# Performance work log

Hardware: AMD Instinct MI355X
Metric: run time of the kernel (lower is better)

Reference implementation:

```python
import jax, jax.numpy as jnp
import numpy as np

NQ = 6          # num_qubits
BS = 3          # basis_size (Pauli x,y,z)
HID = 32        # LSTM hidden size
SNAPS = 16      # max_num_snapshots
BATCH = 1024
DIM = 2 ** NQ   # 64


def _pauli():
    sx = np.array([[0., 1.], [1., 0.]], dtype=np.complex64)
    sy = np.array([[0., -1j], [1j, 0.]], dtype=np.complex64)
    sz = np.array([[1., 0.], [0., -1.]], dtype=np.complex64)
    return np.stack([sx, sy, sz], axis=0)


def setup_inputs():
    key = jax.random.key(0)
    ks = jax.random.split(key, 12)
    snapshot = jax.random.uniform(ks[0], (BATCH, NQ), jnp.float32, -1.0, 1.0)
    basis_comp_vector = jax.nn.softmax(
        jax.random.normal(ks[1], (BATCH, NQ, BS), jnp.float32), axis=-1)
    # valid density matrices: rho = A A^dag / tr
    ar = jax.random.normal(ks[2], (BATCH, DIM, DIM), jnp.float32)
    ai = jax.random.normal(ks[3], (BATCH, DIM, DIM), jnp.float32)
    A = ar + 1j * ai
    rho_c = jnp.einsum('bij,bkj->bik', A, jnp.conj(A))
    tr = jnp.trace(rho_c, axis1=1, axis2=2)[:, None, None]
    rho_c = rho_c / tr
    rho = jnp.stack([jnp.real(rho_c), jnp.imag(rho_c)], axis=1).astype(jnp.float32)
    h0 = jax.random.normal(ks[4], (BATCH, HID), jnp.float32)
    c0 = jax.random.normal(ks[5], (BATCH, HID), jnp.float32)
    in_dim = NQ + NQ * BS
    W_ih = jax.random.normal(ks[6], (4 * HID, in_dim), jnp.float32) * 0.1
    W_hh = jax.random.normal(ks[7], (4 * HID, HID), jnp.float32) * 0.1
    b_ih = jax.random.normal(ks[8], (4 * HID,), jnp.float32) * 0.05
    b_hh = jax.random.normal(ks[9], (4 * HID,), jnp.float32) * 0.05
    Wp = jax.random.normal(ks[10], (NQ, HID, BS), jnp.float32) * 0.1
    bp = jax.random.normal(ks[11], (NQ, BS), jnp.float32) * 0.05
    pauli = _pauli()
    basis_r = jnp.asarray(np.real(pauli), jnp.float32)
    basis_i = jnp.asarray(np.imag(pauli), jnp.float32)
    return {"snapshot": snapshot, "basis_comp_vector": basis_comp_vector,
            "rho": rho, "h0": h0, "c0": c0,
            "W_ih": W_ih, "W_hh": W_hh, "b_ih": b_ih, "b_hh": b_hh,
            "Wp": Wp, "bp": bp, "basis_r": basis_r, "basis_i": basis_i}


def _apply(p, M, axis, b):
    # apply 2x2 batched operator M [b,2,2] on tensor axis `axis` of p [b]+(2,)*2NQ
    pm = jnp.moveaxis(p, axis, 1)
    shp = pm.shape
    out = jnp.einsum('bij,bjr->bir', M, pm.reshape(b, 2, -1)).reshape(shp)
    return jnp.moveaxis(out, 1, axis)


def _measure(rho_t, probs, basis, basis_c, b):
    # sequential single-qubit measurement on the collapsing mixed state
    pc = probs.astype(jnp.complex64)
    M = jnp.einsum('bqs,sij->bqij', pc, basis)    # prob-mixed basis ops
    Mc = jnp.einsum('bqs,sij->bqij', pc, basis_c)
    p = rho_t
    outs = []
    for q in range(NQ):
        p = _apply(p, M[:, q], 1 + q, b)          # row index of qubit q
        p = _apply(p, Mc[:, q], 1 + NQ + q, b)    # col index of qubit q
        tr = jnp.trace(p.reshape(b, DIM, DIM), axis1=1, axis2=2)
        outs.append(jnp.real(tr))                 # measurement value s
        p = p / tr.reshape((b,) + (1,) * (2 * NQ))  # renormalized post-state
    return jnp.stack(outs, axis=1)                 # [b, NQ]


def _forward(snapshot, basis_comp_vector, rho, h0, c0,
             W_ih, W_hh, b_ih, b_hh, Wp, bp, basis_r, basis_i):
    b = snapshot.shape[0]
    basis = (basis_r + 1j * basis_i).astype(jnp.complex64)
    basis_c = jnp.conj(basis)
    rho_t = (rho[:, 0] + 1j * rho[:, 1]).astype(jnp.complex64)
    rho_t = rho_t.reshape((b,) + (2,) * (2 * NQ))

    x = jnp.concatenate([snapshot, basis_comp_vector.reshape(b, -1)], axis=-1)
    feats = [x]
    h, c = h0, c0
    for _ in range(SNAPS - 1):
        # torch LSTMCell: gate order i, f, g, o
        g = x @ W_ih.T + b_ih + h @ W_hh.T + b_hh
        gi, gf, gg, go = jnp.split(g, 4, axis=-1)
        c = jax.nn.sigmoid(gf) * c + jax.nn.sigmoid(gi) * jnp.tanh(gg)
        h = jax.nn.sigmoid(go) * jnp.tanh(c)
        probs = jax.nn.softmax(jnp.einsum('bh,qhs->bqs', h, Wp) + bp, axis=-1)
        # torch.Tensor(snapshot_batch) detaches -> stop_gradient
        snaps = jax.lax.stop_gradient(_measure(rho_t, probs, basis, basis_c, b))
        x = jnp.concatenate([snaps, probs.reshape(b, -1)], axis=-1)
        feats.append(x)

    # classical-shadow reconstruction: kron_q (I + 3 s_q B_q)/2, averaged
    eye2 = jnp.eye(2, dtype=jnp.complex64)
    acc = jnp.zeros((b, DIM, DIM), jnp.complex64)
    last_bv = None
    for xw in feats:
        shadow = xw[:, :NQ]
        bv = xw[:, NQ:].reshape(b, NQ, BS)
        last_bv = bv
        Bq = jnp.einsum('bqs,sij->bqij', bv.astype(jnp.complex64), basis)
        rc = (eye2 + 3.0 * shadow[:, :, None, None].astype(jnp.complex64) * Bq) / 2.0
        k = rc[:, 0]
        dd = 2
        for q in range(1, NQ):  # batched kron chain
            k = jnp.einsum('bij,bkl->bikjl', k, rc[:, q]).reshape(b, dd * 2, dd * 2)
            dd *= 2
        acc = acc + k
    rho_rec = acc / SNAPS
    out = jnp.stack([jnp.real(rho_rec), jnp.imag(rho_rec)], axis=1)
    return out, last_bv


def reference(snapshot, basis_comp_vector, rho, h0, c0,
              W_ih, W_hh, b_ih, b_hh, Wp, bp, basis_r, basis_i):
    return _forward(snapshot, basis_comp_vector, rho, h0, c0,
                    W_ih, W_hh, b_ih, b_hh, Wp, bp, basis_r, basis_i)
```

## Files before the change

kernel.cpp:

```cpp
#include <hip/hip_runtime.h>

#define NQ 6
#define BS 3
#define HID 32
#define SNAPS 16
#define BATCH 1024
#define DIM 64
#define XDIM 24
#define G4 128

#define OFF_WIH  0
#define OFF_WHH  3200
#define OFF_B    7424
#define OFF_WP   7552
#define OFF_BP   8134
#define OFF_KA   0
#define OFF_KB   2048
#define OFF_FEAT 8152
#define OFF_X    8536
#define OFF_H    8560
#define OFF_C    8592
#define OFF_G    8624
#define OFF_P    8752
#define SMEM_FLOATS 8770

__device__ __forceinline__ void rc_entry(float g, float b0, float b1, float b2,
                                         int i, int j, float& re, float& im) {
    if (i == j) { re = 0.5f + (i ? -g * b2 : g * b2); im = 0.0f; }
    else        { re = g * b0;  im = (i ? g * b1 : -g * b1); }
}

__global__ __launch_bounds__(256, 4)
void lstm_shadow_kernel(const float* __restrict__ snapshot,
                        const float* __restrict__ bcv,
                        const float* __restrict__ h0,
                        const float* __restrict__ c0,
                        const float* __restrict__ W_ih,
                        const float* __restrict__ W_hh,
                        const float* __restrict__ b_ih,
                        const float* __restrict__ b_hh,
                        const float* __restrict__ Wp,
                        const float* __restrict__ bp,
                        float* __restrict__ out)
{
    __shared__ float smem[SMEM_FLOATS];
    const int b = blockIdx.x;
    const int t = threadIdx.x;

    float* sWih  = smem + OFF_WIH;
    float* sWhh  = smem + OFF_WHH;
    float* sb    = smem + OFF_B;
    float* sWp   = smem + OFF_WP;
    float* sbp   = smem + OFF_BP;
    float* sfeat = smem + OFF_FEAT;
    float* sx    = smem + OFF_X;
    float* sh    = smem + OFF_H;
    float* sc    = smem + OFF_C;
    float* sg    = smem + OFF_G;
    float* sp    = smem + OFF_P;

    for (int idx = t; idx < G4 * XDIM; idx += 256) {
        int r = idx / XDIM, cc = idx - r * XDIM;
        sWih[r * 25 + cc] = W_ih[idx];
    }
    for (int idx = t; idx < G4 * HID; idx += 256) {
        int r = idx >> 5, cc = idx & 31;
        sWhh[r * 33 + cc] = W_hh[idx];
    }
    if (t < G4) sb[t] = b_ih[t] + b_hh[t];
    for (int idx = t; idx < NQ * HID * BS; idx += 256) {
        int q = idx / 96, rest = idx - q * 96;
        sWp[q * 97 + rest] = Wp[idx];
    }
    if (t < NQ * BS) sbp[t] = bp[t];

    if (t < HID) { sh[t] = h0[b * HID + t]; sc[t] = c0[b * HID + t]; }
    if (t < XDIM) {
        float v = (t < NQ) ? snapshot[b * NQ + t] : bcv[b * (NQ * BS) + (t - NQ)];
        sx[t] = v; sfeat[t] = v;
    }
    __syncthreads();

    for (int step = 0; step < SNAPS - 1; ++step) {
        if (t < G4) {
            float g = sb[t];
            const float* wi = &sWih[t * 25];
            #pragma unroll
            for (int k = 0; k < XDIM; ++k) g += sx[k] * wi[k];
            const float* wh = &sWhh[t * 33];
            #pragma unroll
            for (int k = 0; k < HID; ++k) g += sh[k] * wh[k];
            sg[t] = g;
        }
        __syncthreads();
        if (t < HID) {
            float gi = sg[t], gf = sg[32 + t], gg = sg[64 + t], go = sg[96 + t];
            float si = 1.0f / (1.0f + __expf(-gi));
            float sf = 1.0f / (1.0f + __expf(-gf));
            float so = 1.0f / (1.0f + __expf(-go));
            float cn = sf * sc[t] + si * tanhf(gg);
            sc[t] = cn;
            sh[t] = so * tanhf(cn);
        }
        __syncthreads();
        if (t < NQ * BS) {
            int q = t / 3, s = t - q * 3;
            const float* wp = &sWp[q * 97 + s];
            float l = sbp[t];
            #pragma unroll
            for (int h = 0; h < HID; ++h) l += sh[h] * wp[h * 3];
            sp[t] = l;
        }
        __syncthreads();
        if (t < NQ) {
            float l0 = sp[3 * t], l1 = sp[3 * t + 1], l2 = sp[3 * t + 2];
            float m = fmaxf(l0, fmaxf(l1, l2));
            float e0 = __expf(l0 - m), e1 = __expf(l1 - m), e2 = __expf(l2 - m);
            float inv = 1.0f / (e0 + e1 + e2);
            float p0 = e0 * inv, p1 = e1 * inv, p2 = e2 * inv;
            float snap = p0 * p0 + p1 * p1 + p2 * p2;
            float* fx = &sfeat[(step + 1) * XDIM];
            sx[t] = snap;            fx[t] = snap;
            sx[6 + 3 * t]     = p0;  fx[6 + 3 * t]     = p0;
            sx[6 + 3 * t + 1] = p1;  fx[6 + 3 * t + 1] = p1;
            sx[6 + 3 * t + 2] = p2;  fx[6 + 3 * t + 2] = p2;
        }
        __syncthreads();
    }

    if (t < NQ * BS)
        out[(size_t)BATCH * 8192 + (size_t)b * (NQ * BS) + t] = sfeat[15 * XDIM + 6 + t];

    float* sKA = smem + OFF_KA;
    float* sKB = smem + OFF_KB;
    for (int n = t; n < SNAPS * 64; n += 256) {
        int f = n >> 6, a = n & 63;
        const float* fx = &sfeat[f * XDIM];
        int i0 = (a >> 5) & 1, i1 = (a >> 4) & 1, i2 = (a >> 3) & 1;
        int j0 = (a >> 2) & 1, j1 = (a >> 1) & 1, j2 = a & 1;
        {
            float g0 = 1.5f * fx[0], g1 = 1.5f * fx[1], g2 = 1.5f * fx[2];
            float r0, m0, r1, m1, r2, m2;
            rc_entry(g0, fx[6], fx[7], fx[8],   i0, j0, r0, m0);
            rc_entry(g1, fx[9], fx[10], fx[11], i1, j1, r1, m1);
            rc_entry(g2, fx[12], fx[13], fx[14], i2, j2, r2, m2);
            float pr = r0 * r1 - m0 * m1, pi = r0 * m1 + m0 * r1;
            float qr = pr * r2 - pi * m2, qi = pr * m2 + pi * r2;
            sKA[2 * n]     = qr;
            sKA[2 * n + 1] = qi;
        }
        {
            float g3 = 1.5f * fx[3], g4 = 1.5f * fx[4], g5 = 1.5f * fx[5];
            float r0, m0, r1, m1, r2, m2;
            rc_entry(g3, fx[15], fx[16], fx[17], i0, j0, r0, m0);
            rc_entry(g4, fx[18], fx[19], fx[20], i1, j1, r1, m1);
            rc_entry(g5, fx[21], fx[22], fx[23], i2, j2, r2, m2);
            float pr = r0 * r1 - m0 * m1, pi = r0 * m1 + m0 * r1;
            float qr = pr * r2 - pi * m2, qi = pr * m2 + pi * r2;
            sKB[2 * n]     = qr;
            sKB[2 * n + 1] = qi;
        }
    }
    __syncthreads();

    const int w  = t >> 6;
    const int j  = t & 63;
    const int jA = j >> 3;
    const int jB = j & 7;
    const int beta0 = (w << 3) + jB;
    const int beta1 = ((w + 4) << 3) + jB;

    float accr[16], acci[16];
    #pragma unroll
    for (int e = 0; e < 16; ++e) { accr[e] = 0.0f; acci[e] = 0.0f; }

    #pragma unroll
    for (int f = 0; f < SNAPS; ++f) {
        const float* KAf = &sKA[f * 128];
        const float* KBf = &sKB[f * 128];
        float b0r = KBf[2 * beta0], b0i = KBf[2 * beta0 + 1];
        float b1r = KBf[2 * beta1], b1i = KBf[2 * beta1 + 1];
        #pragma unroll
        for (int m = 0; m < 8; ++m) {
            float ar = KAf[2 * (m * 8 + jA)], ai = KAf[2 * (m * 8 + jA) + 1];
            accr[2 * m]     += ar * b0r - ai * b0i;
            acci[2 * m]     += ar * b0i + ai * b0r;
            accr[2 * m + 1] += ar * b1r - ai * b1i;
            acci[2 * m + 1] += ar * b1i + ai * b1r;
        }
    }

    const float inv16 = 1.0f / 16.0f;
    float* outb = out + (size_t)b * 8192;
    #pragma unroll
    for (int e = 0; e < 16; ++e) {
        int idx = e * 256 + t;
        outb[idx]        = accr[e] * inv16;
        outb[4096 + idx] = acci[e] * inv16;
    }
}

extern "C" void kernel_launch(void* const* d_in, const int* in_sizes, int n_in,
                              void* d_out, int out_size, void* d_ws, size_t ws_size,
                              hipStream_t stream) {
    const float* snapshot = (const float*)d_in[0];
    const float* bcv      = (const float*)d_in[1];
    const float* h0       = (const float*)d_in[3];
    const float* c0       = (const float*)d_in[4];
    const float* W_ih     = (const float*)d_in[5];
    const float* W_hh     = (const float*)d_in[6];
    const float* b_ih     = (const float*)d_in[7];
    const float* b_hh     = (const float*)d_in[8];
    const float* Wp       = (const float*)d_in[9];
    const float* bp       = (const float*)d_in[10];
    float* out = (float*)d_out;

    lstm_shadow_kernel<<<BATCH, 256, 0, stream>>>(
        snapshot, bcv, h0, c0, W_ih, W_hh, b_ih, b_hh, Wp, bp, out);
}
```

Measured before the change: 142.1 us.

## Keep LSTM weights in registers, overlap Kronecker build with recurrence

LSTM gate weights now live in per-thread float4 registers instead of shared memory, which shrinks LDS use and removes the weight-staging loops. Threads 128-255, idle during the recurrence in the old code, now build the Kronecker factors for the previous snapshot while the gate threads work. The cell update, projection and softmax are merged into one 64-thread stage using a wave barrier and shuffles, so each step needs two block barriers instead of four. The Kronecker tables are stored transposed with padding so the accumulate loop can use float4 LDS reads, and tanh uses a fast exp-based form. In exchange, register pressure rises and the fast tanh may differ slightly in precision.

```diff
diff --git a/kernel.cpp b/kernel.cpp
--- a/kernel.cpp
+++ b/kernel.cpp
@@ -5,29 +5,42 @@
 #define HID 32
 #define SNAPS 16
 #define BATCH 1024
-#define DIM 64
 #define XDIM 24
 #define G4 128
 
-#define OFF_WIH  0
-#define OFF_WHH  3200
-#define OFF_B    7424
-#define OFF_WP   7552
-#define OFF_BP   8134
 #define OFF_KA   0
-#define OFF_KB   2048
-#define OFF_FEAT 8152
-#define OFF_X    8536
-#define OFF_H    8560
-#define OFF_C    8592
-#define OFF_G    8624
-#define OFF_P    8752
-#define SMEM_FLOATS 8770
+#define OFF_KB   2560
+#define OFF_WPT  5120
+#define OFF_BP   5768
+#define OFF_FEAT 5788
+#define OFF_X    6172
+#define OFF_H    6196
+#define OFF_G    6228
+#define SMEM_FLOATS 6356
+
+__device__ __forceinline__ float sigm_f(float x) { return 1.0f / (1.0f + __expf(-x)); }
+__device__ __forceinline__ float tanh_f(float x) { return 1.0f - 2.0f / (__expf(2.0f * x) + 1.0f); }
 
 __device__ __forceinline__ void rc_entry(float g, float b0, float b1, float b2,
                                          int i, int j, float& re, float& im) {
     if (i == j) { re = 0.5f + (i ? -g * b2 : g * b2); im = 0.0f; }
     else        { re = g * b0;  im = (i ? g * b1 : -g * b1); }
+}
+
+__device__ __forceinline__ void build_K(const float* fx, int half, int a, float* dst) {
+    int i0 = (a >> 5) & 1, i1 = (a >> 4) & 1, i2 = (a >> 3) & 1;
+    int j0 = (a >> 2) & 1, j1 = (a >> 1) & 1, j2 = a & 1;
+    int q = 3 * half;
+    float g0 = 1.5f * fx[q], g1 = 1.5f * fx[q + 1], g2 = 1.5f * fx[q + 2];
+    const float* bb = fx + 6 + 3 * q;
+    float r0, m0, r1, m1, r2, m2;
+    rc_entry(g0, bb[0], bb[1], bb[2], i0, j0, r0, m0);
+    rc_entry(g1, bb[3], bb[4], bb[5], i1, j1, r1, m1);
+    rc_entry(g2, bb[6], bb[7], bb[8], i2, j2, r2, m2);
+    float pr = r0 * r1 - m0 * m1, pi = r0 * m1 + m0 * r1;
+    float qr = pr * r2 - pi * m2, qi = pr * m2 + pi * r2;
+    int idx = (a & 7) * 20 + 2 * (a >> 3);
+    dst[idx] = qr; dst[idx + 1] = qi;
 }
 
 __global__ __launch_bounds__(256, 4)
@@ -43,123 +56,114 @@
                         const float* __restrict__ bp,
                         float* __restrict__ out)
 {
-    __shared__ float smem[SMEM_FLOATS];
+    __shared__ __align__(16) float smem[SMEM_FLOATS];
     const int b = blockIdx.x;
     const int t = threadIdx.x;
 
-    float* sWih  = smem + OFF_WIH;
-    float* sWhh  = smem + OFF_WHH;
-    float* sb    = smem + OFF_B;
-    float* sWp   = smem + OFF_WP;
+    float* sKA   = smem + OFF_KA;
+    float* sKB   = smem + OFF_KB;
+    float* sWpT  = smem + OFF_WPT;
     float* sbp   = smem + OFF_BP;
     float* sfeat = smem + OFF_FEAT;
     float* sx    = smem + OFF_X;
     float* sh    = smem + OFF_H;
-    float* sc    = smem + OFF_C;
     float* sg    = smem + OFF_G;
-    float* sp    = smem + OFF_P;
-
-    for (int idx = t; idx < G4 * XDIM; idx += 256) {
-        int r = idx / XDIM, cc = idx - r * XDIM;
-        sWih[r * 25 + cc] = W_ih[idx];
-    }
-    for (int idx = t; idx < G4 * HID; idx += 256) {
-        int r = idx >> 5, cc = idx & 31;
-        sWhh[r * 33 + cc] = W_hh[idx];
-    }
-    if (t < G4) sb[t] = b_ih[t] + b_hh[t];
+
+    float4 wih4[6], whh4[8];
+    float breg = 0.0f, creg = 0.0f;
+
+    if (t < G4) {
+        const float4* wi = (const float4*)(W_ih + t * 24);
+        #pragma unroll
+        for (int k = 0; k < 6; ++k) wih4[k] = wi[k];
+        const float4* wh = (const float4*)(W_hh + t * 32);
+        #pragma unroll
+        for (int k = 0; k < 8; ++k) whh4[k] = wh[k];
+        breg = b_ih[t] + b_hh[t];
+    }
     for (int idx = t; idx < NQ * HID * BS; idx += 256) {
-        int q = idx / 96, rest = idx - q * 96;
-        sWp[q * 97 + rest] = Wp[idx];
-    }
-    if (t < NQ * BS) sbp[t] = bp[t];
-
-    if (t < HID) { sh[t] = h0[b * HID + t]; sc[t] = c0[b * HID + t]; }
-    if (t < XDIM) {
-        float v = (t < NQ) ? snapshot[b * NQ + t] : bcv[b * (NQ * BS) + (t - NQ)];
+        int q = idx / 96, r = idx - q * 96;
+        int h = r / 3, s = r - h * 3;
+        sWpT[(q * 3 + s) * 36 + h] = Wp[idx];
+    }
+    if (t < 18) sbp[t] = bp[t];
+    if (t < 32) { sh[t] = h0[b * HID + t]; creg = c0[b * HID + t]; }
+    if (t < 24) {
+        float v = (t < 6) ? snapshot[b * NQ + t] : bcv[b * 18 + (t - 6)];
         sx[t] = v; sfeat[t] = v;
     }
     __syncthreads();
 
     for (int step = 0; step < SNAPS - 1; ++step) {
         if (t < G4) {
-            float g = sb[t];
-            const float* wi = &sWih[t * 25];
+            const float4* sx4 = (const float4*)sx;
+            const float4* sh4 = (const float4*)sh;
+            float ga = breg, gb = 0.0f;
             #pragma unroll
-            for (int k = 0; k < XDIM; ++k) g += sx[k] * wi[k];
-            const float* wh = &sWhh[t * 33];
+            for (int k = 0; k < 6; ++k) {
+                float4 xq = sx4[k];
+                ga += xq.x * wih4[k].x + xq.y * wih4[k].y;
+                gb += xq.z * wih4[k].z + xq.w * wih4[k].w;
+            }
             #pragma unroll
-            for (int k = 0; k < HID; ++k) g += sh[k] * wh[k];
-            sg[t] = g;
+            for (int k = 0; k < 8; ++k) {
+                float4 hq = sh4[k];
+                ga += hq.x * whh4[k].x + hq.y * whh4[k].y;
+                gb += hq.z * whh4[k].z + hq.w * whh4[k].w;
+            }
+            sg[t] = ga + gb;
+        } else {
+            int u = t - G4;
+            const float* fx = &sfeat[step * XDIM];
+            if (u < 64) build_K(fx, 0, u, &sKA[step * 160]);
+            else        build_K(fx, 1, u - 64, &sKB[step * 160]);
         }
         __syncthreads();
-        if (t < HID) {
-            float gi = sg[t], gf = sg[32 + t], gg = sg[64 + t], go = sg[96 + t];
-            float si = 1.0f / (1.0f + __expf(-gi));
-            float sf = 1.0f / (1.0f + __expf(-gf));
-            float so = 1.0f / (1.0f + __expf(-go));
-            float cn = sf * sc[t] + si * tanhf(gg);
-            sc[t] = cn;
-            sh[t] = so * tanhf(cn);
+
+        if (t < 64) {
+            if (t < 32) {
+                float gi = sg[t], gf = sg[32 + t], gg = sg[64 + t], go = sg[96 + t];
+                creg = sigm_f(gf) * creg + sigm_f(gi) * tanh_f(gg);
+                float hnew = sigm_f(go) * tanh_f(creg);
+                sh[t] = hnew;
+            }
+            __builtin_amdgcn_wave_barrier();
+            int row = (t < 18) ? t : 17;
+            const float4* wr  = (const float4*)&sWpT[row * 36];
+            const float4* sh4 = (const float4*)sh;
+            float la = (t < 18) ? sbp[row] : 0.0f, lb = 0.0f;
+            #pragma unroll
+            for (int c2 = 0; c2 < 8; ++c2) {
+                float4 hq = sh4[c2], wq = wr[c2];
+                la += hq.x * wq.x + hq.y * wq.y;
+                lb += hq.z * wq.z + hq.w * wq.w;
+            }
+            float l = la + lb;
+            int q3 = (t < 6) ? 3 * t : 0;
+            float l0 = __shfl(l, q3), l1 = __shfl(l, q3 + 1), l2 = __shfl(l, q3 + 2);
+            if (t < 6) {
+                float m = fmaxf(l0, fmaxf(l1, l2));
+                float e0 = __expf(l0 - m), e1 = __expf(l1 - m), e2 = __expf(l2 - m);
+                float inv = 1.0f / (e0 + e1 + e2);
+                float p0 = e0 * inv, p1 = e1 * inv, p2 = e2 * inv;
+                float snap = p0 * p0 + p1 * p1 + p2 * p2;
+                float* fx2 = &sfeat[(step + 1) * XDIM];
+                sx[t] = snap;              fx2[t] = snap;
+                sx[6 + 3 * t]     = p0;    fx2[6 + 3 * t]     = p0;
+                sx[6 + 3 * t + 1] = p1;    fx2[6 + 3 * t + 1] = p1;
+                sx[6 + 3 * t + 2] = p2;    fx2[6 + 3 * t + 2] = p2;
+            }
         }
         __syncthreads();
-        if (t < NQ * BS) {
-            int q = t / 3, s = t - q * 3;
-            const float* wp = &sWp[q * 97 + s];
-            float l = sbp[t];
-            #pragma unroll
-            for (int h = 0; h < HID; ++h) l += sh[h] * wp[h * 3];
-            sp[t] = l;
-        }
-        __syncthreads();
-        if (t < NQ) {
-            float l0 = sp[3 * t], l1 = sp[3 * t + 1], l2 = sp[3 * t + 2];
-            float m = fmaxf(l0, fmaxf(l1, l2));
-            float e0 = __expf(l0 - m), e1 = __expf(l1 - m), e2 = __expf(l2 - m);
-            float inv = 1.0f / (e0 + e1 + e2);
-            float p0 = e0 * inv, p1 = e1 * inv, p2 = e2 * inv;
-            float snap = p0 * p0 + p1 * p1 + p2 * p2;
-            float* fx = &sfeat[(step + 1) * XDIM];
-            sx[t] = snap;            fx[t] = snap;
-            sx[6 + 3 * t]     = p0;  fx[6 + 3 * t]     = p0;
-            sx[6 + 3 * t + 1] = p1;  fx[6 + 3 * t + 1] = p1;
-            sx[6 + 3 * t + 2] = p2;  fx[6 + 3 * t + 2] = p2;
-        }
-        __syncthreads();
-    }
-
-    if (t < NQ * BS)
-        out[(size_t)BATCH * 8192 + (size_t)b * (NQ * BS) + t] = sfeat[15 * XDIM + 6 + t];
-
-    float* sKA = smem + OFF_KA;
-    float* sKB = smem + OFF_KB;
-    for (int n = t; n < SNAPS * 64; n += 256) {
-        int f = n >> 6, a = n & 63;
-        const float* fx = &sfeat[f * XDIM];
-        int i0 = (a >> 5) & 1, i1 = (a >> 4) & 1, i2 = (a >> 3) & 1;
-        int j0 = (a >> 2) & 1, j1 = (a >> 1) & 1, j2 = a & 1;
-        {
-            float g0 = 1.5f * fx[0], g1 = 1.5f * fx[1], g2 = 1.5f * fx[2];
-            float r0, m0, r1, m1, r2, m2;
-            rc_entry(g0, fx[6], fx[7], fx[8],   i0, j0, r0, m0);
-            rc_entry(g1, fx[9], fx[10], fx[11], i1, j1, r1, m1);
-            rc_entry(g2, fx[12], fx[13], fx[14], i2, j2, r2, m2);
-            float pr = r0 * r1 - m0 * m1, pi = r0 * m1 + m0 * r1;
-            float qr = pr * r2 - pi * m2, qi = pr * m2 + pi * r2;
-            sKA[2 * n]     = qr;
-            sKA[2 * n + 1] = qi;
-        }
-        {
-            float g3 = 1.5f * fx[3], g4 = 1.5f * fx[4], g5 = 1.5f * fx[5];
-            float r0, m0, r1, m1, r2, m2;
-            rc_entry(g3, fx[15], fx[16], fx[17], i0, j0, r0, m0);
-            rc_entry(g4, fx[18], fx[19], fx[20], i1, j1, r1, m1);
-            rc_entry(g5, fx[21], fx[22], fx[23], i2, j2, r2, m2);
-            float pr = r0 * r1 - m0 * m1, pi = r0 * m1 + m0 * r1;
-            float qr = pr * r2 - pi * m2, qi = pr * m2 + pi * r2;
-            sKB[2 * n]     = qr;
-            sKB[2 * n + 1] = qi;
-        }
+    }
+
+    if (t < G4) {
+        const float* fx = &sfeat[15 * XDIM];
+        if (t < 64) build_K(fx, 0, t, &sKA[15 * 160]);
+        else        build_K(fx, 1, t - 64, &sKB[15 * 160]);
+    } else if (t < G4 + 18) {
+        int u = t - G4;
+        out[(size_t)BATCH * 8192 + (size_t)b * 18 + u] = sfeat[15 * XDIM + 6 + u];
     }
     __syncthreads();
 
@@ -167,8 +171,6 @@
     const int j  = t & 63;
     const int jA = j >> 3;
     const int jB = j & 7;
-    const int beta0 = (w << 3) + jB;
-    const int beta1 = ((w + 4) << 3) + jB;
 
     float accr[16], acci[16];
     #pragma unroll
@@ -176,18 +178,24 @@
 
     #pragma unroll
     for (int f = 0; f < SNAPS; ++f) {
-        const float* KAf = &sKA[f * 128];
-        const float* KBf = &sKB[f * 128];
-        float b0r = KBf[2 * beta0], b0i = KBf[2 * beta0 + 1];
-        float b1r = KBf[2 * beta1], b1i = KBf[2 * beta1 + 1];
-        #pragma unroll
-        for (int m = 0; m < 8; ++m) {
-            float ar = KAf[2 * (m * 8 + jA)], ai = KAf[2 * (m * 8 + jA) + 1];
-            accr[2 * m]     += ar * b0r - ai * b0i;
-            acci[2 * m]     += ar * b0i + ai * b0r;
-            accr[2 * m + 1] += ar * b1r - ai * b1i;
-            acci[2 * m + 1] += ar * b1i + ai * b1r;
-        }
+        const float* KAT = &sKA[f * 160 + jA * 20];
+        const float* KBT = &sKB[f * 160 + jB * 20];
+        float4 a0 = ((const float4*)KAT)[0];
+        float4 a1 = ((const float4*)KAT)[1];
+        float4 a2 = ((const float4*)KAT)[2];
+        float4 a3 = ((const float4*)KAT)[3];
+        float b0r = KBT[2 * w],     b0i = KBT[2 * w + 1];
+        float b1r = KBT[2 * w + 8], b1i = KBT[2 * w + 9];
+        #define CMAC(m, ar, ai)                              \
+            accr[2*(m)]   += (ar)*b0r - (ai)*b0i;            \
+            acci[2*(m)]   += (ar)*b0i + (ai)*b0r;            \
+            accr[2*(m)+1] += (ar)*b1r - (ai)*b1i;            \
+            acci[2*(m)+1] += (ar)*b1i + (ai)*b1r;
+        CMAC(0, a0.x, a0.y) CMAC(1, a0.z, a0.w)
+        CMAC(2, a1.x, a1.y) CMAC(3, a1.z, a1.w)
+        CMAC(4, a2.x, a2.y) CMAC(5, a2.z, a2.w)
+        CMAC(6, a3.x, a3.y) CMAC(7, a3.z, a3.w)
+        #undef CMAC
     }
 
     const float inv16 = 1.0f / 16.0f;
```

New measurement: 136.3 us. 1.04x faster.
